# Kernel optimization log

Hardware: AMD Instinct MI355X
Metric: run time of the kernel (lower is better)

Reference implementation:

```python
import jax, jax.numpy as jnp
import numpy as np

H = 16      # multiheads
DH = 64     # head_dim
NEG = 1e12  # mask constant from original code


def setup_inputs() -> dict:
    key = jax.random.key(0)
    ks = jax.random.split(key, 8)
    B, S, D = 8, 1024, 1024
    out_dim = H * DH
    glorot = lambda k, shape: jax.random.uniform(
        k, shape, jnp.float32, -1.0, 1.0) * np.sqrt(6.0 / (shape[0] + shape[1]))
    return {
        "Q_seq": jax.random.normal(ks[0], (B, S, D), jnp.float32),
        "K_seq": jax.random.normal(ks[1], (B, S, D), jnp.float32),
        "V_seq": jax.random.normal(ks[2], (B, S, D), jnp.float32),
        "Q_len": jax.random.randint(ks[3], (B, 1), 0, S, jnp.int32),
        "V_len": jax.random.randint(ks[4], (B, 1), 0, S, jnp.int32),
        "WQ": glorot(ks[5], (D, out_dim)),
        "WK": glorot(ks[6], (D, out_dim)),
        "WV": glorot(ks[7], (D, out_dim)),
    }


def reference(Q_seq, K_seq, V_seq, Q_len, V_len, WQ, WK, WV):
    B, Sq, _ = Q_seq.shape
    Sk = K_seq.shape[1]

    def proj(x, W):  # (B,S,D) -> (B,H,S,DH)
        return (x @ W).reshape(B, x.shape[1], H, DH).transpose(0, 2, 1, 3)

    q = proj(Q_seq, WQ)
    k = proj(K_seq, WK)
    v = proj(V_seq, WV)

    # scores: (B,H,Sq,Sk)
    A = jnp.einsum('bhqd,bhkd->bhqk', q, k) / jnp.sqrt(jnp.float32(DH))

    # key-side length mask (Mask mode='add'): positions >= V_len get -1e12
    kv_valid = (jnp.arange(Sk)[None, :] < V_len).astype(A.dtype)  # (B,Sk)
    A = A - (1.0 - kv_valid)[:, None, None, :] * NEG

    # causal (mask_right=True): upper triangle masked
    causal = jnp.tril(jnp.ones((Sq, Sk), dtype=A.dtype))
    A = A - (1.0 - causal)[None, None, :, :] * NEG

    A = jax.nn.softmax(A, axis=-1)

    O = jnp.einsum('bhqk,bhkd->bhqd', A, v)          # (B,H,Sq,DH)
    O = O.transpose(0, 2, 1, 3).reshape(B, Sq, H * DH)

    # query-side length mask (Mask mode='mul')
    q_valid = (jnp.arange(Sq)[None, :] < Q_len).astype(O.dtype)  # (B,Sq)
    return O * q_valid[:, :, None]
```

## Files before the change

### kernel.cpp

```cpp
#include <hip/hip_runtime.h>
#include <hip/hip_bf16.h>
#include <stdint.h>

#define H_ 16
#define DH_ 64
#define B_ 8
#define S_ 1024
#define D_ 1024

using bf16 = __hip_bfloat16;
typedef __attribute__((ext_vector_type(8))) short bfrag;
typedef __attribute__((ext_vector_type(4))) float facc;
typedef __attribute__((ext_vector_type(4))) float f4;

#define SWZ(r) ((((r) & 7) << 4) ^ (((r) & 8) << 3))
#define SWZP(r) ((((r) >> 1) & 3) << 4)

__device__ __forceinline__ int proj_len(int z, int Ql, int Vl) {
  if (z == 0) return Ql;
  if (z == 1) return Vl;
  return Vl ? Vl : min(Ql + 63, S_);
}

__global__ __launch_bounds__(256) void convert3_f32_bf16(const float* __restrict__ Q,
                                                         const float* __restrict__ K,
                                                         const float* __restrict__ V,
                                                         bf16* __restrict__ o0,
                                                         bf16* __restrict__ o1,
                                                         bf16* __restrict__ o2,
                                                         const int* __restrict__ Qlen,
                                                         const int* __restrict__ Vlen) {
  int z = blockIdx.z;
  int row = blockIdx.x * 2;
  int bb = row >> 10;
  int lrow = row & (S_ - 1);
  int len = proj_len(z, Qlen[bb], Vlen[bb]);
  if ((lrow & ~127) >= len) return;
  const float* in = (z == 0) ? Q : (z == 1) ? K : V;
  bf16* outb = (z == 0) ? o0 : (z == 1) ? o1 : o2;
  int i = blockIdx.x * 256 + threadIdx.x;
  f4 a = ((const f4*)in)[2 * i];
  f4 b = ((const f4*)in)[2 * i + 1];
  alignas(16) bf16 tmp[8];
#pragma unroll
  for (int j = 0; j < 4; ++j) tmp[j] = __float2bfloat16(a[j]);
#pragma unroll
  for (int j = 0; j < 4; ++j) tmp[4 + j] = __float2bfloat16(b[j]);
  *(bfrag*)&outb[8 * i] = *(const bfrag*)tmp;
}

__global__ __launch_bounds__(256) void transpose_w3(const float* __restrict__ WQ,
                                                    const float* __restrict__ WK,
                                                    const float* __restrict__ WV,
                                                    bf16* __restrict__ WT) {
  __shared__ bf16 tile[32][33];
  int z = blockIdx.z;
  const float* W = (z == 0) ? WQ : (z == 1) ? WK : WV;
  float scale = (z == 0) ? 0.125f * 1.44269504f : 1.0f;
  int tx = threadIdx.x & 31, ty = threadIdx.x >> 5;
  int bx = blockIdx.x, by = blockIdx.y;
#pragma unroll
  for (int i = 0; i < 4; ++i) {
    int kk = by * 32 + ty + 8 * i;
    int nn = bx * 32 + tx;
    tile[ty + 8 * i][tx] = __float2bfloat16(W[kk * D_ + nn] * scale);
  }
  __syncthreads();
#pragma unroll
  for (int i = 0; i < 4; ++i) {
    int nn = bx * 32 + ty + 8 * i;
    int kk = by * 32 + tx;
    WT[((size_t)z * 1024 + nn) * D_ + kk] = tile[tx][ty + 8 * i];
  }
}

__global__ __launch_bounds__(256) void proj_gemm(const bf16* __restrict__ A0,
                                                 const bf16* __restrict__ A1,
                                                 const bf16* __restrict__ A2,
                                                 const bf16* __restrict__ Bt,
                                                 bf16* __restrict__ qb,
                                                 bf16* __restrict__ kb,
                                                 bf16* __restrict__ vb,
                                                 const int* __restrict__ Qlen,
                                                 const int* __restrict__ Vlen,
                                                 int zbase) {
  __shared__ __align__(16) bf16 As[128][32];
  __shared__ __align__(16) bf16 Bs[128][32];
  int fid = blockIdx.x;
  int s = fid & 7;
  int y = (fid >> 3) & 7;
  int u = fid >> 6;
  int x, z;
  if (zbase < 0) {
    int q = u * 8 + s;
    z = q % 3;
    x = q / 3;
  } else {
    x = u * 8 + s;
    z = zbase;
  }
  int m0 = x * 128;
  int bb = m0 >> 10;
  int len = proj_len(z, Qlen[bb], Vlen[bb]);
  if ((m0 & (S_ - 1)) >= len) return;
  const bf16* A = (z == 0) ? A0 : (z == 1) ? A1 : A2;
  bf16* outp = (z == 0) ? qb : (z == 1) ? kb : vb;
  int tid = threadIdx.x;
  int lane = tid & 63;
  int wave = tid >> 6;
  int n0 = y * 128;
  int nw = z * 1024 + n0;
  int wm = (wave >> 1) * 64;
  int wn = (wave & 1) * 64;
  int l15 = lane & 15, l4 = lane >> 4;
  int br = lane >> 2;
  int lc = ((lane & 3) ^ ((br >> 1) & 3)) * 8;

  facc acc[4][4] = {};

  for (int k0 = 0; k0 < D_; k0 += 32) {
    __syncthreads();
#pragma unroll
    for (int c = 0; c < 2; ++c) {
      int row = wave * 32 + c * 16;
      __builtin_amdgcn_global_load_lds(
          (const __attribute__((address_space(1))) void*)&A[(size_t)(m0 + row + br) * D_ + k0 + lc],
          (__attribute__((address_space(3))) void*)&As[row][0], 16, 0, 0);
      __builtin_amdgcn_global_load_lds(
          (const __attribute__((address_space(1))) void*)&Bt[(size_t)(nw + row + br) * D_ + k0 + lc],
          (__attribute__((address_space(3))) void*)&Bs[row][0], 16, 0, 0);
    }
    __syncthreads();
    bfrag af[4], bfr[4];
    const char* Ab = (const char*)&As[0][0];
    const char* Bb = (const char*)&Bs[0][0];
#pragma unroll
    for (int i = 0; i < 4; ++i) {
      int row = wm + i * 16 + l15;
      af[i] = *(const bfrag*)(Ab + row * 64 + ((l4 * 16) ^ SWZP(row)));
    }
#pragma unroll
    for (int j = 0; j < 4; ++j) {
      int row = wn + j * 16 + l15;
      bfr[j] = *(const bfrag*)(Bb + row * 64 + ((l4 * 16) ^ SWZP(row)));
    }
#pragma unroll
    for (int i = 0; i < 4; ++i)
#pragma unroll
      for (int j = 0; j < 4; ++j)
        acc[i][j] = __builtin_amdgcn_mfma_f32_16x16x32_bf16(af[i], bfr[j], acc[i][j], 0, 0, 0);
  }

  bool vmode = (z == 2);
#pragma unroll
  for (int i = 0; i < 4; ++i)
#pragma unroll
    for (int j = 0; j < 4; ++j)
#pragma unroll
      for (int r = 0; r < 4; ++r) {
        int gm = m0 + wm + i * 16 + l4 * 4 + r;
        int gn = n0 + wn + j * 16 + l15;
        int b = gm >> 10, sr = gm & (S_ - 1);
        int h = gn >> 6, dh = gn & 63;
        bf16 val = __float2bfloat16(acc[i][j][r]);
        if (!vmode)
          outp[(((size_t)b * H_ + h) * S_ + sr) * DH_ + dh] = val;
        else
          outp[(((size_t)b * H_ + h) * DH_ + dh) * S_ + sr] = val;
      }
}

__global__ __launch_bounds__(256) void attn_fwd(const bf16* __restrict__ q,
                                                const bf16* __restrict__ k,
                                                const bf16* __restrict__ vT,
                                                const int* __restrict__ Qlen,
                                                const int* __restrict__ Vlen,
                                                float* __restrict__ out) {
  __shared__ __align__(16) bf16 Kt[2][64 * 64];
  __shared__ __align__(16) bf16 Vt[2][64 * 64];
  int tid = threadIdx.x, lane = tid & 63, wave = tid >> 6;
  int bid = blockIdx.x;
  int h = bid & 15, b = (bid >> 4) & 7;
  int qt = 15 - (bid >> 7);
  int q0b = qt * 64;
  int q0 = q0b + wave * 16;
  int Vl = Vlen[b], Ql = Qlen[b];
  int l15 = lane & 15, g = lane >> 4;
  int qrow = q0 + l15;

  if (q0b >= Ql) {
    f4 zz = {0.f, 0.f, 0.f, 0.f};
#pragma unroll
    for (int t = 0; t < 4; ++t)
      *(f4*)&out[((size_t)b * S_ + qrow) * (H_ * DH_) + h * DH_ + t * 16 + g * 4] = zz;
    return;
  }

  const bf16* qp = q + (size_t)(b * H_ + h) * S_ * DH_;
  const bf16* kp = k + (size_t)(b * H_ + h) * S_ * DH_;
  const bf16* vp = vT + (size_t)(b * H_ + h) * DH_ * S_;
  bool vzero = (Vl == 0);

  int jlim = vzero ? (qrow + 1) : min(qrow + 1, Vl);
  int wmin = vzero ? (q0 + 1) : min(q0 + 1, Vl);
  int wmax = vzero ? (q0 + 16) : min(q0 + 16, Vl);
  if (q0 >= Ql) wmax = 0;

  bfrag qf0 = *(const bfrag*)&qp[(q0 + l15) * DH_ + g * 8];
  bfrag qf1 = *(const bfrag*)&qp[(q0 + l15) * DH_ + 32 + g * 8];

  facc o[4] = {};
  float mrow = -1e30f, lrow = 0.f;

  int kendb = q0b + 64;
  if (!vzero) kendb = kendb < Vl ? kendb : Vl;
  int nblk = (kendb + 63) >> 6;

  int krow0 = 8 * (l15 >> 2) + (l15 & 3);
  int sr0 = wave * 16 + (lane >> 3);
  int sbb = (lane & 7) * 16;

  auto stage = [&](int buf, int kbase) {
    int r0 = sr0, r1 = sr0 + 8;
    const char* kg0 = (const char*)(kp + (size_t)(kbase + r0) * DH_) + (sbb ^ SWZ(r0));
    const char* kg1 = (const char*)(kp + (size_t)(kbase + r1) * DH_) + (sbb ^ SWZ(r1));
    const char* vg0 = (const char*)(vp + (size_t)r0 * S_ + kbase) + (sbb ^ SWZ(r0));
    const char* vg1 = (const char*)(vp + (size_t)r1 * S_ + kbase) + (sbb ^ SWZ(r1));
    char* kl = (char*)&Kt[buf][0] + wave * 2048;
    char* vl = (char*)&Vt[buf][0] + wave * 2048;
    __builtin_amdgcn_global_load_lds((const __attribute__((address_space(1))) void*)kg0,
        (__attribute__((address_space(3))) void*)kl, 16, 0, 0);
    __builtin_amdgcn_global_load_lds((const __attribute__((address_space(1))) void*)kg1,
        (__attribute__((address_space(3))) void*)(kl + 1024), 16, 0, 0);
    __builtin_amdgcn_global_load_lds((const __attribute__((address_space(1))) void*)vg0,
        (__attribute__((address_space(3))) void*)vl, 16, 0, 0);
    __builtin_amdgcn_global_load_lds((const __attribute__((address_space(1))) void*)vg1,
        (__attribute__((address_space(3))) void*)(vl + 1024), 16, 0, 0);
  };

  stage(0, 0);
  __syncthreads();

  for (int kb = 0; kb < nblk; ++kb) {
    int cur = kb & 1;
    int kbase = kb * 64;
    if (kb + 1 < nblk) stage(1 - cur, (kb + 1) * 64);

    if (kbase < wmax) {
      facc z[4] = {};
      if (!vzero) {
#pragma unroll
        for (int gg = 0; gg < 2; ++gg) {
          int ra = gg * 32 + krow0;
          int rb = ra + 4;
          const char* Kc = (const char*)&Kt[cur][0];
          bfrag a0 = *(const bfrag*)(Kc + ra * 128 + ((g * 16) ^ SWZ(ra)));
          bfrag a1 = *(const bfrag*)(Kc + ra * 128 + ((g * 16 + 64) ^ SWZ(ra)));
          z[2 * gg] = __builtin_amdgcn_mfma_f32_16x16x32_bf16(a0, qf0, z[2 * gg], 0, 0, 0);
          z[2 * gg] = __builtin_amdgcn_mfma_f32_16x16x32_bf16(a1, qf1, z[2 * gg], 0, 0, 0);
          bfrag a2 = *(const bfrag*)(Kc + rb * 128 + ((g * 16) ^ SWZ(rb)));
          bfrag a3 = *(const bfrag*)(Kc + rb * 128 + ((g * 16 + 64) ^ SWZ(rb)));
          z[2 * gg + 1] = __builtin_amdgcn_mfma_f32_16x16x32_bf16(a2, qf0, z[2 * gg + 1], 0, 0, 0);
          z[2 * gg + 1] = __builtin_amdgcn_mfma_f32_16x16x32_bf16(a3, qf1, z[2 * gg + 1], 0, 0, 0);
        }
      }

      float sv[16];
#pragma unroll
      for (int gg = 0; gg < 2; ++gg)
#pragma unroll
        for (int c = 0; c < 4; ++c) {
          sv[8 * gg + c] = z[2 * gg][c];
          sv[8 * gg + 4 + c] = z[2 * gg + 1][c];
        }
      if (kbase + 64 > wmin) {
#pragma unroll
        for (int gg = 0; gg < 2; ++gg)
#pragma unroll
          for (int c = 0; c < 8; ++c) {
            int j = kbase + 32 * gg + 8 * g + c;
            if (j >= jlim) sv[8 * gg + c] = -1e12f;
          }
      }

      float mxl = sv[0];
#pragma unroll
      for (int c = 1; c < 16; ++c) mxl = fmaxf(mxl, sv[c]);

      if (!__all(mxl <= mrow + 8.0f)) {
        float mx = fmaxf(mxl, __shfl_xor(mxl, 16, 64));
        mx = fmaxf(mx, __shfl_xor(mx, 32, 64));
        float nm = fmaxf(mrow, mx);
        float sc = exp2f(mrow - nm);
        lrow *= sc;
#pragma unroll
        for (int t = 0; t < 4; ++t)
#pragma unroll
          for (int r = 0; r < 4; ++r) o[t][r] *= sc;
        mrow = nm;
      }

      alignas(16) bf16 pb[16];
      float ss = 0.f;
#pragma unroll
      for (int c = 0; c < 16; ++c) {
        float pv = exp2f(sv[c] - mrow);
        ss += pv;
        pb[c] = __float2bfloat16(pv);
      }
      ss += __shfl_xor(ss, 16, 64);
      ss += __shfl_xor(ss, 32, 64);
      lrow += ss;

      bfrag pf0 = *(const bfrag*)&pb[0];
      bfrag pf1 = *(const bfrag*)&pb[8];
      const char* Vc = (const char*)&Vt[cur][0];
#pragma unroll
      for (int t = 0; t < 4; ++t) {
        int d = t * 16 + l15;
        bfrag vf0 = *(const bfrag*)(Vc + d * 128 + ((g * 16) ^ SWZ(d)));
        bfrag vf1 = *(const bfrag*)(Vc + d * 128 + ((g * 16 + 64) ^ SWZ(d)));
        o[t] = __builtin_amdgcn_mfma_f32_16x16x32_bf16(vf0, pf0, o[t], 0, 0, 0);
        o[t] = __builtin_amdgcn_mfma_f32_16x16x32_bf16(vf1, pf1, o[t], 0, 0, 0);
      }
    }

    __syncthreads();
  }

  float inv = 1.0f / lrow;
  if (qrow >= Ql) inv = 0.f;
#pragma unroll
  for (int t = 0; t < 4; ++t) {
    f4 ov;
#pragma unroll
    for (int r = 0; r < 4; ++r) ov[r] = o[t][r] * inv;
    *(f4*)&out[((size_t)b * S_ + qrow) * (H_ * DH_) + h * DH_ + t * 16 + g * 4] = ov;
  }
}

extern "C" void kernel_launch(void* const* d_in, const int* in_sizes, int n_in,
                              void* d_out, int out_size, void* d_ws, size_t ws_size,
                              hipStream_t stream) {
  const float* Qs = (const float*)d_in[0];
  const float* Ks = (const float*)d_in[1];
  const float* Vs = (const float*)d_in[2];
  const int* Qlen = (const int*)d_in[3];
  const int* Vlen = (const int*)d_in[4];
  const float* WQ = (const float*)d_in[5];
  const float* WK = (const float*)d_in[6];
  const float* WV = (const float*)d_in[7];
  float* out = (float*)d_out;

  char* ws = (char*)d_ws;
  const size_t MB = 1024 * 1024;
  bf16* wT = (bf16*)(ws + 0 * MB);
  dim3 tb(256);
  const int CVT_GRID = (B_ * S_ * D_) / (8 * 256);

  transpose_w3<<<dim3(32, 32, 3), tb, 0, stream>>>(WQ, WK, WV, wT);

  if (ws_size >= 102 * MB) {
    bf16* xc0 = (bf16*)(ws + 6 * MB);
    bf16* xc1 = (bf16*)(ws + 22 * MB);
    bf16* xc2 = (bf16*)(ws + 38 * MB);
    bf16* qb  = (bf16*)(ws + 54 * MB);
    bf16* kb  = (bf16*)(ws + 70 * MB);
    bf16* vb  = (bf16*)(ws + 86 * MB);
    convert3_f32_bf16<<<dim3(CVT_GRID, 1, 3), tb, 0, stream>>>(Qs, Ks, Vs, xc0, xc1, xc2,
                                                               Qlen, Vlen);
    proj_gemm<<<dim3(1536, 1, 1), tb, 0, stream>>>(xc0, xc1, xc2, wT, qb, kb, vb,
                                                   Qlen, Vlen, -1);
    attn_fwd<<<dim3(B_ * H_ * (S_ / 64)), tb, 0, stream>>>(qb, kb, vb, Qlen, Vlen, out);
  } else {
    bf16* xc = (bf16*)(ws + 6 * MB);
    bf16* qb = (bf16*)(ws + 22 * MB);
    bf16* kb = (bf16*)(ws + 38 * MB);
    bf16* vb = (bf16*)(ws + 54 * MB);
    convert3_f32_bf16<<<dim3(CVT_GRID, 1, 1), tb, 0, stream>>>(Qs, Ks, Vs, xc, xc, xc,
                                                               Qlen, Vlen);
    proj_gemm<<<dim3(512, 1, 1), tb, 0, stream>>>(xc, xc, xc, wT, qb, kb, vb, Qlen, Vlen, 0);
    convert3_f32_bf16<<<dim3(CVT_GRID, 1, 1), tb, 0, stream>>>(Ks, Ks, Ks, xc, xc, xc,
                                                               Qlen, Vlen);
    proj_gemm<<<dim3(512, 1, 1), tb, 0, stream>>>(xc, xc, xc, wT, qb, kb, vb, Qlen, Vlen, 1);
    convert3_f32_bf16<<<dim3(CVT_GRID, 1, 1), tb, 0, stream>>>(Vs, Vs, Vs, xc, xc, xc,
                                                               Qlen, Vlen);
    proj_gemm<<<dim3(512, 1, 1), tb, 0, stream>>>(xc, xc, xc, wT, qb, kb, vb, Qlen, Vlen, 2);
    attn_fwd<<<dim3(B_ * H_ * (S_ / 64)), tb, 0, stream>>>(qb, kb, vb, Qlen, Vlen, out);
  }
}
```

Measured before the change: 113.7 us.

## Fuse fp32-to-bf16 input conversion into projection GEMM tile loads

Drops the separate conversion kernel and has the projection GEMM load fp32 activation tiles straight into swizzled LDS, converting to bf16 while building MFMA fragments. This removes a full bf16 write and re-read of the activations plus one kernel launch, and makes the workspace layout the same regardless of workspace size. In exchange the GEMM moves twice as many bytes from global memory into LDS per A tile, uses more LDS, and converts every tile redundantly across the eight N-blocks. The block ordering also changes so the y (N) tiles of one M tile run together.

Measured after the change: 126.7 us. +11.4%, slower.

```diff
diff --git a/kernel.cpp b/kernel.cpp
--- a/kernel.cpp
+++ b/kernel.cpp
@@ -20,33 +20,6 @@
   if (z == 0) return Ql;
   if (z == 1) return Vl;
   return Vl ? Vl : min(Ql + 63, S_);
-}
-
-__global__ __launch_bounds__(256) void convert3_f32_bf16(const float* __restrict__ Q,
-                                                         const float* __restrict__ K,
-                                                         const float* __restrict__ V,
-                                                         bf16* __restrict__ o0,
-                                                         bf16* __restrict__ o1,
-                                                         bf16* __restrict__ o2,
-                                                         const int* __restrict__ Qlen,
-                                                         const int* __restrict__ Vlen) {
-  int z = blockIdx.z;
-  int row = blockIdx.x * 2;
-  int bb = row >> 10;
-  int lrow = row & (S_ - 1);
-  int len = proj_len(z, Qlen[bb], Vlen[bb]);
-  if ((lrow & ~127) >= len) return;
-  const float* in = (z == 0) ? Q : (z == 1) ? K : V;
-  bf16* outb = (z == 0) ? o0 : (z == 1) ? o1 : o2;
-  int i = blockIdx.x * 256 + threadIdx.x;
-  f4 a = ((const f4*)in)[2 * i];
-  f4 b = ((const f4*)in)[2 * i + 1];
-  alignas(16) bf16 tmp[8];
-#pragma unroll
-  for (int j = 0; j < 4; ++j) tmp[j] = __float2bfloat16(a[j]);
-#pragma unroll
-  for (int j = 0; j < 4; ++j) tmp[4 + j] = __float2bfloat16(b[j]);
-  *(bfrag*)&outb[8 * i] = *(const bfrag*)tmp;
 }
 
 __global__ __launch_bounds__(256) void transpose_w3(const float* __restrict__ WQ,
@@ -74,36 +47,26 @@
   }
 }
 
-__global__ __launch_bounds__(256) void proj_gemm(const bf16* __restrict__ A0,
-                                                 const bf16* __restrict__ A1,
-                                                 const bf16* __restrict__ A2,
+__global__ __launch_bounds__(256) void proj_gemm(const float* __restrict__ A0,
+                                                 const float* __restrict__ A1,
+                                                 const float* __restrict__ A2,
                                                  const bf16* __restrict__ Bt,
                                                  bf16* __restrict__ qb,
                                                  bf16* __restrict__ kb,
                                                  bf16* __restrict__ vb,
                                                  const int* __restrict__ Qlen,
-                                                 const int* __restrict__ Vlen,
-                                                 int zbase) {
-  __shared__ __align__(16) bf16 As[128][32];
+                                                 const int* __restrict__ Vlen) {
+  __shared__ __align__(16) float Asf[128][32];
   __shared__ __align__(16) bf16 Bs[128][32];
   int fid = blockIdx.x;
-  int s = fid & 7;
-  int y = (fid >> 3) & 7;
-  int u = fid >> 6;
-  int x, z;
-  if (zbase < 0) {
-    int q = u * 8 + s;
-    z = q % 3;
-    x = q / 3;
-  } else {
-    x = u * 8 + s;
-    z = zbase;
-  }
+  int y = fid & 7;
+  int z = (fid >> 3) % 3;
+  int x = fid / 24;
   int m0 = x * 128;
   int bb = m0 >> 10;
   int len = proj_len(z, Qlen[bb], Vlen[bb]);
   if ((m0 & (S_ - 1)) >= len) return;
-  const bf16* A = (z == 0) ? A0 : (z == 1) ? A1 : A2;
+  const float* A = (z == 0) ? A0 : (z == 1) ? A1 : A2;
   bf16* outp = (z == 0) ? qb : (z == 1) ? kb : vb;
   int tid = threadIdx.x;
   int lane = tid & 63;
@@ -115,29 +78,47 @@
   int l15 = lane & 15, l4 = lane >> 4;
   int br = lane >> 2;
   int lc = ((lane & 3) ^ ((br >> 1) & 3)) * 8;
+  int ar = lane >> 3;
+  int as = (lane & 7) * 16;
 
   facc acc[4][4] = {};
 
   for (int k0 = 0; k0 < D_; k0 += 32) {
     __syncthreads();
+#pragma unroll
+    for (int c = 0; c < 4; ++c) {
+      int rowb = wave * 32 + c * 8;
+      int row = rowb + ar;
+      const char* src = (const char*)&A[(size_t)(m0 + row) * D_ + k0] + (as ^ SWZ(row));
+      char* dst = (char*)&Asf[0][0] + rowb * 128;
+      __builtin_amdgcn_global_load_lds((const __attribute__((address_space(1))) void*)src,
+                                       (__attribute__((address_space(3))) void*)dst, 16, 0, 0);
+    }
 #pragma unroll
     for (int c = 0; c < 2; ++c) {
       int row = wave * 32 + c * 16;
       __builtin_amdgcn_global_load_lds(
-          (const __attribute__((address_space(1))) void*)&A[(size_t)(m0 + row + br) * D_ + k0 + lc],
-          (__attribute__((address_space(3))) void*)&As[row][0], 16, 0, 0);
-      __builtin_amdgcn_global_load_lds(
           (const __attribute__((address_space(1))) void*)&Bt[(size_t)(nw + row + br) * D_ + k0 + lc],
           (__attribute__((address_space(3))) void*)&Bs[row][0], 16, 0, 0);
     }
     __syncthreads();
+
     bfrag af[4], bfr[4];
-    const char* Ab = (const char*)&As[0][0];
+    const char* Ab = (const char*)&Asf[0][0];
     const char* Bb = (const char*)&Bs[0][0];
 #pragma unroll
     for (int i = 0; i < 4; ++i) {
       int row = wm + i * 16 + l15;
-      af[i] = *(const bfrag*)(Ab + row * 64 + ((l4 * 16) ^ SWZP(row)));
+      const char* rp = Ab + row * 128;
+      f4 lo = *(const f4*)(rp + ((l4 * 32) ^ SWZ(row)));
+      f4 hi = *(const f4*)(rp + ((l4 * 32 + 16) ^ SWZ(row)));
+      alignas(16) bf16 t[8];
+#pragma unroll
+      for (int j = 0; j < 4; ++j) {
+        t[j] = __float2bfloat16(lo[j]);
+        t[4 + j] = __float2bfloat16(hi[j]);
+      }
+      af[i] = *(const bfrag*)t;
     }
 #pragma unroll
     for (int j = 0; j < 4; ++j) {
@@ -355,37 +336,12 @@
   char* ws = (char*)d_ws;
   const size_t MB = 1024 * 1024;
   bf16* wT = (bf16*)(ws + 0 * MB);
+  bf16* qb = (bf16*)(ws + 6 * MB);
+  bf16* kb = (bf16*)(ws + 22 * MB);
+  bf16* vb = (bf16*)(ws + 38 * MB);
   dim3 tb(256);
-  const int CVT_GRID = (B_ * S_ * D_) / (8 * 256);
 
   transpose_w3<<<dim3(32, 32, 3), tb, 0, stream>>>(WQ, WK, WV, wT);
-
-  if (ws_size >= 102 * MB) {
-    bf16* xc0 = (bf16*)(ws + 6 * MB);
-    bf16* xc1 = (bf16*)(ws + 22 * MB);
-    bf16* xc2 = (bf16*)(ws + 38 * MB);
-    bf16* qb  = (bf16*)(ws + 54 * MB);
-    bf16* kb  = (bf16*)(ws + 70 * MB);
-    bf16* vb  = (bf16*)(ws + 86 * MB);
-    convert3_f32_bf16<<<dim3(CVT_GRID, 1, 3), tb, 0, stream>>>(Qs, Ks, Vs, xc0, xc1, xc2,
-                                                               Qlen, Vlen);
-    proj_gemm<<<dim3(1536, 1, 1), tb, 0, stream>>>(xc0, xc1, xc2, wT, qb, kb, vb,
-                                                   Qlen, Vlen, -1);
-    attn_fwd<<<dim3(B_ * H_ * (S_ / 64)), tb, 0, stream>>>(qb, kb, vb, Qlen, Vlen, out);
-  } else {
-    bf16* xc = (bf16*)(ws + 6 * MB);
-    bf16* qb = (bf16*)(ws + 22 * MB);
-    bf16* kb = (bf16*)(ws + 38 * MB);
-    bf16* vb = (bf16*)(ws + 54 * MB);
-    convert3_f32_bf16<<<dim3(CVT_GRID, 1, 1), tb, 0, stream>>>(Qs, Ks, Vs, xc, xc, xc,
-                                                               Qlen, Vlen);
-    proj_gemm<<<dim3(512, 1, 1), tb, 0, stream>>>(xc, xc, xc, wT, qb, kb, vb, Qlen, Vlen, 0);
-    convert3_f32_bf16<<<dim3(CVT_GRID, 1, 1), tb, 0, stream>>>(Ks, Ks, Ks, xc, xc, xc,
-                                                               Qlen, Vlen);
-    proj_gemm<<<dim3(512, 1, 1), tb, 0, stream>>>(xc, xc, xc, wT, qb, kb, vb, Qlen, Vlen, 1);
-    convert3_f32_bf16<<<dim3(CVT_GRID, 1, 1), tb, 0, stream>>>(Vs, Vs, Vs, xc, xc, xc,
-                                                               Qlen, Vlen);
-    proj_gemm<<<dim3(512, 1, 1), tb, 0, stream>>>(xc, xc, xc, wT, qb, kb, vb, Qlen, Vlen, 2);
-    attn_fwd<<<dim3(B_ * H_ * (S_ / 64)), tb, 0, stream>>>(qb, kb, vb, Qlen, Vlen, out);
-  }
-}
+  proj_gemm<<<dim3(1536, 1, 1), tb, 0, stream>>>(Qs, Ks, Vs, wT, qb, kb, vb, Qlen, Vlen);
+  attn_fwd<<<dim3(B_ * H_ * (S_ / 64)), tb, 0, stream>>>(qb, kb, vb, Qlen, Vlen, out);
+}
```
